# Performance work log

Hardware: AMD Instinct MI355X
Metric: run time of the kernel (lower is better)

The kernel has to match this reference:

```python
import jax, jax.numpy as jnp
import numpy as np
from jax import lax

EPS = 1e-5  # torch BatchNorm2d default


def setup_inputs() -> dict:
    key = jax.random.key(0)
    k1, k2 = jax.random.split(key)
    x = jax.random.normal(k1, (8, 32, 28, 28), dtype=jnp.float32)
    # AdderConv.param: [out_channel, in_channel, k, k], init ~ N(0,1)
    W = jax.random.normal(k2, (64, 32, 3, 3), dtype=jnp.float32)
    # BatchNorm2d affine params at init
    gamma = jnp.ones((64,), dtype=jnp.float32)
    beta = jnp.zeros((64,), dtype=jnp.float32)
    return {"x": x, "W": W, "gamma": gamma, "beta": beta}


def _adder(patches, Wc):
    # patches: [N, K, Ho, Wo] with K = C*kh*kw (channel-major, matching torch unfold)
    # Wc: [O, K]
    # AdderNet: out[n,o,ho,wo] = -sum_k |patches[n,k,ho,wo] - Wc[o,k]|
    diff = patches[:, None, :, :, :] - Wc[None, :, :, None, None]  # [N,O,K,Ho,Wo]
    return -jnp.abs(diff).sum(axis=2)  # [N,O,Ho,Wo]


def reference(x, W, gamma, beta):
    O, C, kh, kw = W.shape
    # im2col, same layout as torch.nn.functional.unfold: feature dim = C*kh*kw
    patches = lax.conv_general_dilated_patches(
        x, (kh, kw), window_strides=(1, 1), padding=[(1, 1), (1, 1)]
    )  # [N, C*kh*kw, Ho, Wo]
    Wc = W.reshape(O, C * kh * kw)
    out = _adder(patches, Wc)  # [N, O, Ho, Wo]
    # BatchNorm2d, training mode (batch statistics, biased variance)
    mean = out.mean(axis=(0, 2, 3), keepdims=True)
    var = out.var(axis=(0, 2, 3), keepdims=True)
    y = (out - mean) * lax.rsqrt(var + EPS)
    return y * gamma[None, :, None, None] + beta[None, :, None, None]
```

## Files before the change

kernel.cpp:

```cpp
#include <hip/hip_runtime.h>

#define NB   8
#define CIN  32
#define HH   28
#define WW   28
#define OC   64
#define HWSZ (HH*WW)
#define TOTAL (NB*OC*HWSZ)
#define CNT  (NB*HWSZ)

#define KH   16
#define TROWS 4
#define TCOLS 30
#define TSZ  (KH*TROWS*TCOLS)

#define CPW  2

__global__ __launch_bounds__(256) void adder_kernel(
    const float* __restrict__ x, const float* __restrict__ Wt,
    float* __restrict__ raw01)
{
    __shared__ float xs[TSZ];
    const int t     = threadIdx.x;
    const int bid   = blockIdx.x;
    const int khalf = bid & 1;
    const int chgrp = (bid >> 1) & 7;
    const int rp    = (bid >> 4) % 14;
    const int n     = bid / (16 * 14);
    const int h0    = rp * 2;
    const int c0    = khalf * KH;

    for (int i = t; i < TSZ; i += 256) {
        int cc  = i / (TROWS*TCOLS);
        int rem = i % (TROWS*TCOLS);
        int r   = rem / TCOLS;
        int col = rem % TCOLS;
        int hh  = h0 - 1 + r;
        int ww  = col - 1;
        float v = 0.0f;
        if (hh >= 0 && hh < HH && ww >= 0 && ww < WW)
            v = x[((n*CIN + (c0+cc))*HH + hh)*WW + ww];
        xs[i] = v;
    }
    __syncthreads();

    const int lane  = t & 63;
    const int g     = __builtin_amdgcn_readfirstlane(t >> 6);
    const bool valid = lane < 56;
    const int p     = valid ? lane : 0;
    const int pr    = p / WW;
    const int pw    = p % WW;
    const int o_base = chgrp*8 + g*CPW;

    float acc[CPW];
    #pragma unroll
    for (int oo = 0; oo < CPW; ++oo) acc[oo] = 0.0f;

    float xr[9];
    {
        int b0 = pr*TCOLS + pw;
        #pragma unroll
        for (int dr = 0; dr < 3; ++dr)
            #pragma unroll
            for (int dc = 0; dc < 3; ++dc)
                xr[dr*3+dc] = xs[b0 + dr*TCOLS + dc];
    }

    for (int cc = 0; cc < KH; ++cc) {
        float xn[9];
        if (cc + 1 < KH) {
            int b2 = ((cc+1)*TROWS + pr)*TCOLS + pw;
            #pragma unroll
            for (int dr = 0; dr < 3; ++dr)
                #pragma unroll
                for (int dc = 0; dc < 3; ++dc)
                    xn[dr*3+dc] = xs[b2 + dr*TCOLS + dc];
        }
        #pragma unroll
        for (int oo = 0; oo < CPW; ++oo) {
            const float* wp = Wt + ((o_base + oo)*CIN + (c0 + cc))*9;
            #pragma unroll
            for (int j = 0; j < 9; ++j)
                acc[oo] += __builtin_fabsf(xr[j] - wp[j]);
        }
        if (cc + 1 < KH) {
            #pragma unroll
            for (int j = 0; j < 9; ++j) xr[j] = xn[j];
        }
    }

    if (valid) {
        float* rawh = raw01 + khalf * TOTAL;
        #pragma unroll
        for (int oo = 0; oo < CPW; ++oo)
            rawh[((n*OC + o_base + oo)*HH + (h0 + pr))*WW + pw] = -acc[oo];
    }
}

__global__ __launch_bounds__(256) void stats_kernel(
    const float* __restrict__ raw01,
    const float* __restrict__ gamma, const float* __restrict__ beta,
    float* __restrict__ sc)
{
    const int o = blockIdx.x;
    const int t = threadIdx.x;
    const float4* r0 = (const float4*)raw01;
    const float4* r1 = (const float4*)(raw01 + TOTAL);
    double s = 0.0, s2 = 0.0;
    for (int i4 = t; i4 < CNT/4; i4 += 256) {
        int nn  = i4 / (HWSZ/4);
        int pos = i4 % (HWSZ/4);
        int idx = (nn*OC + o)*(HWSZ/4) + pos;
        float4 a = r0[idx];
        float4 b = r1[idx];
        float vx = a.x + b.x, vy = a.y + b.y, vz = a.z + b.z, vw = a.w + b.w;
        s  += (double)vx + (double)vy + (double)vz + (double)vw;
        s2 += (double)vx*vx + (double)vy*vy + (double)vz*vz + (double)vw*vw;
    }
    #pragma unroll
    for (int off = 32; off >= 1; off >>= 1) {
        s  += __shfl_xor(s,  off, 64);
        s2 += __shfl_xor(s2, off, 64);
    }
    __shared__ double ls[4], ls2[4];
    const int lane = t & 63, w = t >> 6;
    if (lane == 0) { ls[w] = s; ls2[w] = s2; }
    __syncthreads();
    if (t == 0) {
        double S  = ls[0] + ls[1] + ls[2] + ls[3];
        double S2 = ls2[0] + ls2[1] + ls2[2] + ls2[3];
        double mean = S * (1.0 / CNT);
        double var  = S2 * (1.0 / CNT) - mean * mean;
        double inv  = 1.0 / sqrt(var + 1e-5);
        double scl  = (double)gamma[o] * inv;
        sc[o]       = (float)scl;
        sc[64 + o]  = (float)((double)beta[o] - mean * scl);
    }
}

__global__ __launch_bounds__(256) void bn_kernel(
    const float* __restrict__ raw01, const float* __restrict__ sc,
    float* __restrict__ out)
{
    int i4 = blockIdx.x * 256 + threadIdx.x;
    if (i4 >= TOTAL/4) return;
    int o = (i4 / (HWSZ/4)) & (OC - 1);
    float s = sc[o];
    float b = sc[64 + o];
    float4 a0 = ((const float4*)raw01)[i4];
    float4 a1 = ((const float4*)(raw01 + TOTAL))[i4];
    float4 v;
    v.x = (a0.x + a1.x) * s + b;
    v.y = (a0.y + a1.y) * s + b;
    v.z = (a0.z + a1.z) * s + b;
    v.w = (a0.w + a1.w) * s + b;
    ((float4*)out)[i4] = v;
}

extern "C" void kernel_launch(void* const* d_in, const int* in_sizes, int n_in,
                              void* d_out, int out_size, void* d_ws, size_t ws_size,
                              hipStream_t stream) {
    const float* x     = (const float*)d_in[0];
    const float* Wt    = (const float*)d_in[1];
    const float* gamma = (const float*)d_in[2];
    const float* beta  = (const float*)d_in[3];
    float* out = (float*)d_out;

    float* sc    = (float*)d_ws;
    float* raw01 = (float*)((char*)d_ws + 4096);

    adder_kernel<<<NB*14*8*2, 256, 0, stream>>>(x, Wt, raw01);
    stats_kernel<<<OC, 256, 0, stream>>>(raw01, gamma, beta, sc);
    bn_kernel<<<(TOTAL/4 + 255) / 256, 256, 0, stream>>>(raw01, sc, out);
}
```

Before: 78.07 us.

## Fuse BN statistics into adder kernel via atomics and drop K-split

Removes the input-channel split so each block accumulates all 32 channels and writes one raw buffer instead of two partial halves. BN sum and sum-of-squares are computed with wave reductions and double atomics inside the adder kernel, which eliminates the separate stats kernel. The BN kernel now derives scale and shift per element from the accumulated sums. The trade-off is fewer blocks (448 instead of 1792) with more work each, plus a memset launch and atomic contention.

```diff
diff --git a/kernel.cpp b/kernel.cpp
--- a/kernel.cpp
+++ b/kernel.cpp
@@ -9,37 +9,34 @@
 #define TOTAL (NB*OC*HWSZ)
 #define CNT  (NB*HWSZ)
 
-#define KH   16
 #define TROWS 4
-#define TCOLS 30
-#define TSZ  (KH*TROWS*TCOLS)
+#define TCOLS 32
+#define TSZ  (CIN*TROWS*TCOLS)
 
-#define CPW  2
+#define CPW  4
+#define CHGRP 4
 
-__global__ __launch_bounds__(256) void adder_kernel(
+__global__ __launch_bounds__(256) void adder_stats_kernel(
     const float* __restrict__ x, const float* __restrict__ Wt,
-    float* __restrict__ raw01)
+    float* __restrict__ raw, double* __restrict__ S, double* __restrict__ S2)
 {
     __shared__ float xs[TSZ];
     const int t     = threadIdx.x;
     const int bid   = blockIdx.x;
-    const int khalf = bid & 1;
-    const int chgrp = (bid >> 1) & 7;
-    const int rp    = (bid >> 4) % 14;
-    const int n     = bid / (16 * 14);
+    const int chgrp = bid & (CHGRP-1);
+    const int rp    = (bid >> 2) % 14;
+    const int n     = bid / (CHGRP * 14);
     const int h0    = rp * 2;
-    const int c0    = khalf * KH;
 
     for (int i = t; i < TSZ; i += 256) {
-        int cc  = i / (TROWS*TCOLS);
-        int rem = i % (TROWS*TCOLS);
-        int r   = rem / TCOLS;
-        int col = rem % TCOLS;
+        int cc  = i >> 7;
+        int r   = (i >> 5) & 3;
+        int col = i & 31;
         int hh  = h0 - 1 + r;
         int ww  = col - 1;
         float v = 0.0f;
-        if (hh >= 0 && hh < HH && ww >= 0 && ww < WW)
-            v = x[((n*CIN + (c0+cc))*HH + hh)*WW + ww];
+        if (hh >= 0 && hh < HH && (unsigned)ww < (unsigned)WW)
+            v = x[((n*CIN + cc)*HH + hh)*WW + ww];
         xs[i] = v;
     }
     __syncthreads();
@@ -50,110 +47,73 @@
     const int p     = valid ? lane : 0;
     const int pr    = p / WW;
     const int pw    = p % WW;
-    const int o_base = chgrp*8 + g*CPW;
+    const int o_base = chgrp*16 + g*CPW;
+    const int b0    = pr*TCOLS + pw;
 
     float acc[CPW];
     #pragma unroll
     for (int oo = 0; oo < CPW; ++oo) acc[oo] = 0.0f;
 
-    float xr[9];
-    {
-        int b0 = pr*TCOLS + pw;
+    for (int cc = 0; cc < CIN; ++cc) {
+        float xr[9];
         #pragma unroll
         for (int dr = 0; dr < 3; ++dr)
             #pragma unroll
             for (int dc = 0; dc < 3; ++dc)
-                xr[dr*3+dc] = xs[b0 + dr*TCOLS + dc];
-    }
-
-    for (int cc = 0; cc < KH; ++cc) {
-        float xn[9];
-        if (cc + 1 < KH) {
-            int b2 = ((cc+1)*TROWS + pr)*TCOLS + pw;
-            #pragma unroll
-            for (int dr = 0; dr < 3; ++dr)
-                #pragma unroll
-                for (int dc = 0; dc < 3; ++dc)
-                    xn[dr*3+dc] = xs[b2 + dr*TCOLS + dc];
-        }
+                xr[dr*3+dc] = xs[(cc << 7) + b0 + (dr << 5) + dc];
         #pragma unroll
         for (int oo = 0; oo < CPW; ++oo) {
-            const float* wp = Wt + ((o_base + oo)*CIN + (c0 + cc))*9;
+            const float* wp = Wt + ((o_base + oo)*CIN + cc)*9;
             #pragma unroll
             for (int j = 0; j < 9; ++j)
                 acc[oo] += __builtin_fabsf(xr[j] - wp[j]);
         }
-        if (cc + 1 < KH) {
-            #pragma unroll
-            for (int j = 0; j < 9; ++j) xr[j] = xn[j];
-        }
     }
 
     if (valid) {
-        float* rawh = raw01 + khalf * TOTAL;
         #pragma unroll
         for (int oo = 0; oo < CPW; ++oo)
-            rawh[((n*OC + o_base + oo)*HH + (h0 + pr))*WW + pw] = -acc[oo];
+            raw[((n*OC + o_base + oo)*HH + (h0 + pr))*WW + pw] = -acc[oo];
     }
-}
 
-__global__ __launch_bounds__(256) void stats_kernel(
-    const float* __restrict__ raw01,
-    const float* __restrict__ gamma, const float* __restrict__ beta,
-    float* __restrict__ sc)
-{
-    const int o = blockIdx.x;
-    const int t = threadIdx.x;
-    const float4* r0 = (const float4*)raw01;
-    const float4* r1 = (const float4*)(raw01 + TOTAL);
-    double s = 0.0, s2 = 0.0;
-    for (int i4 = t; i4 < CNT/4; i4 += 256) {
-        int nn  = i4 / (HWSZ/4);
-        int pos = i4 % (HWSZ/4);
-        int idx = (nn*OC + o)*(HWSZ/4) + pos;
-        float4 a = r0[idx];
-        float4 b = r1[idx];
-        float vx = a.x + b.x, vy = a.y + b.y, vz = a.z + b.z, vw = a.w + b.w;
-        s  += (double)vx + (double)vy + (double)vz + (double)vw;
-        s2 += (double)vx*vx + (double)vy*vy + (double)vz*vz + (double)vw*vw;
-    }
     #pragma unroll
-    for (int off = 32; off >= 1; off >>= 1) {
-        s  += __shfl_xor(s,  off, 64);
-        s2 += __shfl_xor(s2, off, 64);
-    }
-    __shared__ double ls[4], ls2[4];
-    const int lane = t & 63, w = t >> 6;
-    if (lane == 0) { ls[w] = s; ls2[w] = s2; }
-    __syncthreads();
-    if (t == 0) {
-        double S  = ls[0] + ls[1] + ls[2] + ls[3];
-        double S2 = ls2[0] + ls2[1] + ls2[2] + ls2[3];
-        double mean = S * (1.0 / CNT);
-        double var  = S2 * (1.0 / CNT) - mean * mean;
-        double inv  = 1.0 / sqrt(var + 1e-5);
-        double scl  = (double)gamma[o] * inv;
-        sc[o]       = (float)scl;
-        sc[64 + o]  = (float)((double)beta[o] - mean * scl);
+    for (int oo = 0; oo < CPW; ++oo) {
+        float v  = valid ? -acc[oo] : 0.0f;
+        float s  = v;
+        float s2 = v * v;
+        #pragma unroll
+        for (int off = 32; off >= 1; off >>= 1) {
+            s  += __shfl_xor(s,  off, 64);
+            s2 += __shfl_xor(s2, off, 64);
+        }
+        if (lane == 0) {
+            atomicAdd(&S [o_base + oo], (double)s);
+            atomicAdd(&S2[o_base + oo], (double)s2);
+        }
     }
 }
 
 __global__ __launch_bounds__(256) void bn_kernel(
-    const float* __restrict__ raw01, const float* __restrict__ sc,
+    const float* __restrict__ raw,
+    const double* __restrict__ S, const double* __restrict__ S2,
+    const float* __restrict__ gamma, const float* __restrict__ beta,
     float* __restrict__ out)
 {
     int i4 = blockIdx.x * 256 + threadIdx.x;
     if (i4 >= TOTAL/4) return;
     int o = (i4 / (HWSZ/4)) & (OC - 1);
-    float s = sc[o];
-    float b = sc[64 + o];
-    float4 a0 = ((const float4*)raw01)[i4];
-    float4 a1 = ((const float4*)(raw01 + TOTAL))[i4];
+    double mean = S[o]  * (1.0 / CNT);
+    double var  = S2[o] * (1.0 / CNT) - mean * mean;
+    double inv  = 1.0 / sqrt(var + 1e-5);
+    double gs   = (double)gamma[o] * inv;
+    float scl   = (float)gs;
+    float sh    = (float)((double)beta[o] - mean * gs);
+    float4 a = ((const float4*)raw)[i4];
     float4 v;
-    v.x = (a0.x + a1.x) * s + b;
-    v.y = (a0.y + a1.y) * s + b;
-    v.z = (a0.z + a1.z) * s + b;
-    v.w = (a0.w + a1.w) * s + b;
+    v.x = a.x * scl + sh;
+    v.y = a.y * scl + sh;
+    v.z = a.z * scl + sh;
+    v.w = a.w * scl + sh;
     ((float4*)out)[i4] = v;
 }
 
@@ -166,10 +126,11 @@
     const float* beta  = (const float*)d_in[3];
     float* out = (float*)d_out;
 
-    float* sc    = (float*)d_ws;
-    float* raw01 = (float*)((char*)d_ws + 4096);
+    double* S   = (double*)d_ws;
+    double* S2  = S + 64;
+    float*  raw = (float*)((char*)d_ws + 4096);
 
-    adder_kernel<<<NB*14*8*2, 256, 0, stream>>>(x, Wt, raw01);
-    stats_kernel<<<OC, 256, 0, stream>>>(raw01, gamma, beta, sc);
-    bn_kernel<<<(TOTAL/4 + 255) / 256, 256, 0, stream>>>(raw01, sc, out);
+    hipMemsetAsync(d_ws, 0, 1024, stream);
+    adder_stats_kernel<<<NB*14*CHGRP, 256, 0, stream>>>(x, Wt, raw, S, S2);
+    bn_kernel<<<(TOTAL/4 + 255) / 256, 256, 0, stream>>>(raw, S, S2, gamma, beta, out);
 }
```

New measurement: 102.3 us. 1.31x slower.

## Fuse BN stats and normalize into one kernel caching channel in LDS

Applied to the files above, without the earlier changes.

Merges the stats and normalize kernels into a single per-channel kernel. The summed channel values (6272 floats, about 25KB) are kept in shared memory so the normalize pass reads them from LDS rather than re-reading both partial buffers from global memory. This removes one kernel launch and one full read of the raw data. The cost is that the normalize pass now runs on only 64 blocks, which limits parallelism on the write side.

```diff
diff --git a/kernel.cpp b/kernel.cpp
--- a/kernel.cpp
+++ b/kernel.cpp
@@ -97,32 +97,38 @@
     }
 }
 
-__global__ __launch_bounds__(256) void stats_kernel(
+__global__ __launch_bounds__(256) void statsbn_kernel(
     const float* __restrict__ raw01,
     const float* __restrict__ gamma, const float* __restrict__ beta,
-    float* __restrict__ sc)
+    float* __restrict__ out)
 {
+    __shared__ float vbuf[CNT];
+    __shared__ double ls[4], ls2[4];
+    __shared__ float sb[2];
     const int o = blockIdx.x;
     const int t = threadIdx.x;
     const float4* r0 = (const float4*)raw01;
     const float4* r1 = (const float4*)(raw01 + TOTAL);
+
     double s = 0.0, s2 = 0.0;
+    #pragma unroll 2
     for (int i4 = t; i4 < CNT/4; i4 += 256) {
         int nn  = i4 / (HWSZ/4);
         int pos = i4 % (HWSZ/4);
         int idx = (nn*OC + o)*(HWSZ/4) + pos;
         float4 a = r0[idx];
         float4 b = r1[idx];
-        float vx = a.x + b.x, vy = a.y + b.y, vz = a.z + b.z, vw = a.w + b.w;
-        s  += (double)vx + (double)vy + (double)vz + (double)vw;
-        s2 += (double)vx*vx + (double)vy*vy + (double)vz*vz + (double)vw*vw;
+        float4 v;
+        v.x = a.x + b.x; v.y = a.y + b.y; v.z = a.z + b.z; v.w = a.w + b.w;
+        ((float4*)vbuf)[i4] = v;
+        s  += (double)v.x + (double)v.y + (double)v.z + (double)v.w;
+        s2 += (double)v.x*v.x + (double)v.y*v.y + (double)v.z*v.z + (double)v.w*v.w;
     }
     #pragma unroll
     for (int off = 32; off >= 1; off >>= 1) {
         s  += __shfl_xor(s,  off, 64);
         s2 += __shfl_xor(s2, off, 64);
     }
-    __shared__ double ls[4], ls2[4];
     const int lane = t & 63, w = t >> 6;
     if (lane == 0) { ls[w] = s; ls2[w] = s2; }
     __syncthreads();
@@ -133,28 +139,24 @@
         double var  = S2 * (1.0 / CNT) - mean * mean;
         double inv  = 1.0 / sqrt(var + 1e-5);
         double scl  = (double)gamma[o] * inv;
-        sc[o]       = (float)scl;
-        sc[64 + o]  = (float)((double)beta[o] - mean * scl);
+        sb[0] = (float)scl;
+        sb[1] = (float)((double)beta[o] - mean * scl);
     }
-}
-
-__global__ __launch_bounds__(256) void bn_kernel(
-    const float* __restrict__ raw01, const float* __restrict__ sc,
-    float* __restrict__ out)
-{
-    int i4 = blockIdx.x * 256 + threadIdx.x;
-    if (i4 >= TOTAL/4) return;
-    int o = (i4 / (HWSZ/4)) & (OC - 1);
-    float s = sc[o];
-    float b = sc[64 + o];
-    float4 a0 = ((const float4*)raw01)[i4];
-    float4 a1 = ((const float4*)(raw01 + TOTAL))[i4];
-    float4 v;
-    v.x = (a0.x + a1.x) * s + b;
-    v.y = (a0.y + a1.y) * s + b;
-    v.z = (a0.z + a1.z) * s + b;
-    v.w = (a0.w + a1.w) * s + b;
-    ((float4*)out)[i4] = v;
+    __syncthreads();
+    const float scl = sb[0], sh = sb[1];
+    #pragma unroll 2
+    for (int i4 = t; i4 < CNT/4; i4 += 256) {
+        int nn  = i4 / (HWSZ/4);
+        int pos = i4 % (HWSZ/4);
+        int idx = (nn*OC + o)*(HWSZ/4) + pos;
+        float4 v = ((const float4*)vbuf)[i4];
+        float4 y;
+        y.x = v.x * scl + sh;
+        y.y = v.y * scl + sh;
+        y.z = v.z * scl + sh;
+        y.w = v.w * scl + sh;
+        ((float4*)out)[idx] = y;
+    }
 }
 
 extern "C" void kernel_launch(void* const* d_in, const int* in_sizes, int n_in,
@@ -166,10 +168,8 @@
     const float* beta  = (const float*)d_in[3];
     float* out = (float*)d_out;
 
-    float* sc    = (float*)d_ws;
     float* raw01 = (float*)((char*)d_ws + 4096);
 
     adder_kernel<<<NB*14*8*2, 256, 0, stream>>>(x, Wt, raw01);
-    stats_kernel<<<OC, 256, 0, stream>>>(raw01, gamma, beta, sc);
-    bn_kernel<<<(TOTAL/4 + 255) / 256, 256, 0, stream>>>(raw01, sc, out);
+    statsbn_kernel<<<OC, 256, 0, stream>>>(raw01, gamma, beta, out);
 }
```

New measurement: 74.73 us, median of 2. 1.04x faster.
